# Optimization experiments

Measured on AMD Instinct MI355X. Metric: run time of the kernel, lower is better.

The kernel has to match this reference:

```python
import jax, jax.numpy as jnp
import numpy as np

# ---------- constants ----------
EPS = 1e-5
_rng = np.random.default_rng(0)
_P = _rng.normal(size=(8, 3))
_P /= np.linalg.norm(_P, axis=1, keepdims=True)

def _y2_np(p):
    x, y, z = p[:, 0], p[:, 1], p[:, 2]
    return np.stack([x * y, y * z, 3 * z * z - 1, x * z, x * x - y * y], axis=-1)

_A2 = np.linalg.pinv(_y2_np(_P)).astype(np.float32)  # [5,8]
P_C = jnp.asarray(_P.astype(np.float32))
A2_C = jnp.asarray(_A2)
NORM_CONST = np.float32(1.0 / np.sqrt(20.0))  # avg_num_neighbors ** -0.5
# res update (buffer zeros, not learnable): sigmoid(0)=0.5
_U = 0.5
C_OLD = np.float32(1.0 / np.sqrt(_U * _U + 1.0))
C_NEW = np.float32(_U * C_OLD)


def _y2(p):  # real l=2 monomial basis on unit vectors
    x, y, z = p[..., 0], p[..., 1], p[..., 2]
    return jnp.stack([x * y, y * z, 3.0 * z * z - 1.0, x * z, x * x - y * y], axis=-1)


def _frame(v):  # [E,3] -> R [E,3,3] with R @ v_hat = z
    n = v / jnp.linalg.norm(v, axis=-1, keepdims=True)
    z = jnp.array([0.0, 0.0, 1.0], v.dtype)
    xa = jnp.array([1.0, 0.0, 0.0], v.dtype)
    a = jnp.where(jnp.abs(n[:, 2:3]) < 0.99, z, xa)
    e1 = jnp.cross(a, n)
    e1 = e1 / jnp.linalg.norm(e1, axis=-1, keepdims=True)
    e2 = jnp.cross(n, e1)
    return jnp.stack([e1, e2, n], axis=1)


def _wigner_d2(R):  # [E,3,3] -> D2 [E,5,5] via sample-point fit
    pts = jnp.einsum('pj,eij->epi', P_C, R)  # R @ p_k, [E,8,3]
    M = _y2(pts)  # [E,8,5] = Y_P @ D^T
    Dt = jnp.einsum('ap,epb->eab', A2_C, M)  # [E,5,5]
    return jnp.swapaxes(Dt, 1, 2)


def _sln(x, w0, b0, w1, w2):  # separable equivariant layernorm, 32x0e+16x1e+8x2e
    s = x[:, :32]
    v1 = x[:, 32:80].reshape(-1, 16, 3)
    v2 = x[:, 80:120].reshape(-1, 8, 5)
    mu = jnp.mean(s, axis=-1, keepdims=True)
    var = jnp.mean((s - mu) ** 2, axis=-1, keepdims=True)
    s = (s - mu) * jax.lax.rsqrt(var + EPS) * w0 + b0
    var1 = jnp.mean(v1 ** 2, axis=(1, 2))  # degree-balanced component variance
    var2 = jnp.mean(v2 ** 2, axis=(1, 2))
    inv = jax.lax.rsqrt(0.5 * (var1 + var2) + EPS)[:, None, None]
    v1 = v1 * inv * w1[None, :, None]
    v2 = v2 * inv * w2[None, :, None]
    return jnp.concatenate([s, v1.reshape(-1, 48), v2.reshape(-1, 40)], axis=-1)


def _ir_linear(x, W0, b0, W1, W2):  # irreps-wise linear 32x0e+16x1e+8x2e -> same
    s = x[:, :32] @ (W0 / np.sqrt(32.0)) + b0
    v1 = jnp.einsum('eui,uv->evi', x[:, 32:80].reshape(-1, 16, 3), W1) / np.sqrt(16.0)
    v2 = jnp.einsum('eui,uv->evi', x[:, 80:120].reshape(-1, 8, 5), W2) / np.sqrt(8.0)
    return jnp.concatenate([s, v1.reshape(-1, 48), v2.reshape(-1, 40)], axis=-1)


def _so2(x_cat, R, D2f, D2b, w):  # SO2 linear with per-edge dynamic weights
    E = x_cat.shape[0]
    w0 = w[:, :8960].reshape(E, 112, 80)
    w1r = w[:, 8960:10112].reshape(E, 48, 24)
    w1i = w[:, 10112:11264].reshape(E, 48, 24)
    w2r = w[:, 11264:11392].reshape(E, 16, 8)
    w2i = w[:, 11392:11520].reshape(E, 16, 8)
    # split concatenated [in + hidden] blocks
    s = jnp.concatenate([x_cat[:, :32], x_cat[:, 120:152]], axis=-1)  # [E,64]
    v1 = jnp.concatenate([x_cat[:, 32:80].reshape(E, 16, 3),
                          x_cat[:, 152:200].reshape(E, 16, 3)], axis=1)  # [E,32,3]
    v2 = jnp.concatenate([x_cat[:, 80:120].reshape(E, 8, 5),
                          x_cat[:, 200:240].reshape(E, 16 // 2, 5)], axis=1)  # [E,16,5]
    # rotate into edge-aligned frame
    v1 = jnp.einsum('eij,euj->eui', R, v1)
    v2 = jnp.einsum('eij,euj->eui', D2f, v2)
    in0 = jnp.concatenate([s, v1[:, :, 1], v2[:, :, 2]], axis=-1)   # m=0, [E,112]
    inn1 = jnp.concatenate([v1[:, :, 0], v2[:, :, 1]], axis=-1)     # m=-1, [E,48]
    inp1 = jnp.concatenate([v1[:, :, 2], v2[:, :, 3]], axis=-1)     # m=+1
    inn2 = v2[:, :, 0]  # m=-2
    inp2 = v2[:, :, 4]  # m=+2
    out0 = jnp.einsum('ei,eio->eo', in0, w0) / np.sqrt(112.0)
    op1 = (jnp.einsum('ei,eio->eo', inp1, w1r) - jnp.einsum('ei,eio->eo', inn1, w1i)) / np.sqrt(48.0)
    on1 = (jnp.einsum('ei,eio->eo', inn1, w1r) + jnp.einsum('ei,eio->eo', inp1, w1i)) / np.sqrt(48.0)
    op2 = (jnp.einsum('ei,eio->eo', inp2, w2r) - jnp.einsum('ei,eio->eo', inn2, w2i)) / np.sqrt(16.0)
    on2 = (jnp.einsum('ei,eio->eo', inn2, w2r) + jnp.einsum('ei,eio->eo', inp2, w2i)) / np.sqrt(16.0)
    s_out = out0[:, :56]
    y1 = jnp.stack([on1[:, :16], out0[:, 56:72], op1[:, :16]], axis=-1)  # [E,16,3]
    y2o = jnp.stack([on2, on1[:, 16:24], out0[:, 72:80], op1[:, 16:24], op2], axis=-1)  # [E,8,5]
    # rotate back
    y1 = jnp.einsum('eij,euj->eui', jnp.swapaxes(R, 1, 2), y1)
    y2o = jnp.einsum('eij,euj->eui', D2b, y2o)
    return jnp.concatenate([s_out, y1.reshape(E, 48), y2o.reshape(E, 40)], axis=-1)  # [E,144]


def _gate(m):  # 32x0e scalars | 24x0e gates | 16x1e+8x2e gated
    s = jax.nn.silu(m[:, :32])
    g = jax.nn.sigmoid(m[:, 32:56])
    v1 = m[:, 56:104].reshape(-1, 16, 3) * g[:, :16, None]
    v2 = m[:, 104:144].reshape(-1, 8, 5) * g[:, 16:24, None]
    return jnp.concatenate([s, v1.reshape(-1, 48), v2.reshape(-1, 40)], axis=-1)


def _env(m, we):  # E3ElementLinear: per-mul elementwise weights
    s = m[:, :32] * we[:, :32]
    v1 = m[:, 32:80].reshape(-1, 16, 3) * we[:, 32:48, None]
    v2 = m[:, 80:120].reshape(-1, 8, 5) * we[:, 48:56, None]
    return jnp.concatenate([s, v1.reshape(-1, 48), v2.reshape(-1, 40)], axis=-1)


def setup_inputs() -> dict:
    key = jax.random.key(0)
    ks = jax.random.split(key, 16)
    N, E, L = 512, 10240, 128
    inp = {
        'latents': jax.random.normal(ks[0], (E, L), jnp.float32),
        'node_features': jax.random.normal(ks[1], (N, 120), jnp.float32),
        'hidden_features': jax.random.normal(ks[2], (E, 120), jnp.float32),
        'node_onehot': jnp.ones((N, 16), jnp.float32),
        'edge_vector': jax.random.normal(ks[3], (E, 3), jnp.float32),
        'W_tp': jax.random.normal(ks[4], (L, 11520), jnp.float32),
        'W_env': jax.random.normal(ks[5], (L, 56), jnp.float32),
        'sln_w0': jnp.ones((32,), jnp.float32),
        'sln_b0': jnp.zeros((32,), jnp.float32),
        'sln_w1': jnp.ones((16,), jnp.float32),
        'sln_w2': jnp.ones((8,), jnp.float32),
        'Wp0': jax.random.normal(ks[6], (32, 32), jnp.float32),
        'bp0': jnp.zeros((32,), jnp.float32),
        'Wp1': jax.random.normal(ks[7], (16, 16), jnp.float32),
        'Wp2': jax.random.normal(ks[8], (8, 8), jnp.float32),
        'Wr0': jax.random.normal(ks[9], (32, 32), jnp.float32),
        'br0': jnp.zeros((32,), jnp.float32),
        'Wr1': jax.random.normal(ks[10], (16, 16), jnp.float32),
        'Wr2': jax.random.normal(ks[11], (8, 8), jnp.float32),
        'atom_type': jax.random.randint(ks[12], (N,), 0, 10, jnp.int32),
        'edge_index': jax.random.randint(ks[13], (2, E), 0, N, jnp.int32),
        'active_edges': jnp.arange(E, dtype=jnp.int32),
    }
    return inp


def reference(latents, node_features, hidden_features, node_onehot, edge_vector,
              W_tp, W_env, sln_w0, sln_b0, sln_w1, sln_w2,
              Wp0, bp0, Wp1, Wp2, Wr0, br0, Wr1, Wr2,
              atom_type, edge_index, active_edges):
    n_nodes = node_features.shape[0]
    center = edge_index[0][active_edges]
    nf = _sln(node_features, sln_w0, sln_b0, sln_w1, sln_w2)
    x_cat = jnp.concatenate([nf[center], hidden_features], axis=-1)  # [E,240]
    v = edge_vector[active_edges]
    R = _frame(v)
    D2f = _wigner_d2(R)
    D2b = _wigner_d2(jnp.swapaxes(R, 1, 2))
    wdyn = latents @ (W_tp / np.sqrt(128.0))  # per-edge dynamic SO2 weights
    msg = _so2(x_cat, R, D2f, D2b, wdyn)
    msg = _gate(msg)
    msg = _ir_linear(msg, Wp0, bp0, Wp1, Wp2)
    wenv = latents[active_edges] @ (W_env / np.sqrt(128.0))
    weighted = _env(msg, wenv)
    new_nf = jax.ops.segment_sum(weighted, center, num_segments=n_nodes)
    new_nf = new_nf * NORM_CONST
    res = _ir_linear(node_features, Wr0, br0, Wr1, Wr2)
    return C_NEW * new_nf + C_OLD * res
```

## Files before the change

### kernel.cpp

```cpp
#include <hip/hip_runtime.h>
#include <math.h>

#define E_TOT   10240
#define N_NODES 512
#define NCOL    11520

typedef unsigned short ushort_t;
typedef unsigned int   uint_t;
typedef __bf16 bf16x8 __attribute__((ext_vector_type(8)));
typedef float  f32x4  __attribute__((ext_vector_type(4)));

constexpr float EPSF        = 1e-5f;
constexpr float INV_SQRT128 = 0.08838834764831845f;
constexpr float INV_SQRT112 = 0.09449111825230681f;
constexpr float INV_SQRT48  = 0.14433756729740643f;
constexpr float INV_SQRT32  = 0.17677669529663687f;
constexpr float INV_SQRT16  = 0.25f;
constexpr float INV_SQRT8   = 0.35355339059327373f;
constexpr float SC0 = INV_SQRT128 * INV_SQRT112;
constexpr float SC1 = INV_SQRT128 * INV_SQRT48;
constexpr float SC2 = INV_SQRT128 * INV_SQRT16;
constexpr float C_OLD_ = 0.8944271909999159f;
constexpr float C_NEW_ = 0.4472135954999579f;
constexpr float NORMC  = 0.22360679774997896f;

__device__ __forceinline__ float wsum(float v) {
#pragma unroll
  for (int off = 32; off > 0; off >>= 1) v += __shfl_xor(v, off, 64);
  return v;
}

__device__ __forceinline__ ushort_t f2bf(float x) {
  uint_t u = __float_as_uint(x);
  u = (u + 0x7fffu + ((u >> 16) & 1u)) >> 16;
  return (ushort_t)u;
}

__device__ __forceinline__ void wigner5(const float q[9], float D[25]) {
  const float q0x=q[0],q0y=q[1],q0z=q[2];
  const float q1x=q[3],q1y=q[4],q1z=q[5];
  const float q2x=q[6],q2y=q[7],q2z=q[8];
  D[0]  = q0x*q1y + q1x*q0y;
  D[1]  = q0y*q1z + q1y*q0z;
  D[2]  = 0.5f*(q0z*q1z);
  D[3]  = q0x*q1z + q1x*q0z;
  D[4]  = 0.5f*(q0x*q1x - q0y*q1y);
  D[5]  = q1x*q2y + q2x*q1y;
  D[6]  = q1y*q2z + q2y*q1z;
  D[7]  = 0.5f*(q1z*q2z);
  D[8]  = q1x*q2z + q2x*q1z;
  D[9]  = 0.5f*(q1x*q2x - q1y*q2y);
  D[10] = 6.f*q2x*q2y;
  D[11] = 6.f*q2y*q2z;
  D[12] = 0.5f*(3.f*q2z*q2z - 1.f);
  D[13] = 6.f*q2x*q2z;
  D[14] = 1.5f*(q2x*q2x - q2y*q2y);
  D[15] = q0x*q2y + q2x*q0y;
  D[16] = q0y*q2z + q2y*q0z;
  D[17] = 0.5f*(q0z*q2z);
  D[18] = q0x*q2z + q2x*q0z;
  D[19] = 0.5f*(q0x*q2x - q0y*q2y);
  D[20] = 2.f*(q0x*q0y - q1x*q1y);
  D[21] = 2.f*(q0y*q0z - q1y*q1z);
  D[22] = 0.5f*(q0z*q0z - q1z*q1z);
  D[23] = 2.f*(q0x*q0z - q1x*q1z);
  D[24] = 0.5f*((q0x*q0x - q1x*q1x) - (q0y*q0y - q1y*q1y));
}

__global__ void k0_latpack(const float* __restrict__ lat,
                           ushort_t* __restrict__ lath, ushort_t* __restrict__ latl) {
  int idx = blockIdx.x*256 + threadIdx.x;
  if (idx >= E_TOT*128) return;
  float x = lat[idx];
  ushort_t h = f2bf(x);
  float hf = __uint_as_float(((uint_t)h) << 16);
  lath[idx] = h;
  latl[idx] = f2bf(x - hf);
}

__global__ void k_pack(const float* __restrict__ Wtp, ushort_t* __restrict__ Wp) {
  const int nt = blockIdx.x;
  const int t = threadIdx.x;
  const int kc = t >> 6, lane = t & 63;
  const int m = lane & 15, kg = lane >> 4;
  int col, tt;
  if (nt < 560)      { col = nt/112; tt = nt - col*112; }
  else if (nt < 608) { col = 5;  tt = nt-560; }
  else if (nt < 632) { col = 6;  tt = nt-608; }
  else if (nt < 680) { col = 7;  tt = nt-632; }
  else if (nt < 704) { col = 8;  tt = nt-680; }
  else if (nt < 712) { col = 9;  tt = nt-704; }
  else               { col = 10; tt = nt-712; }
  int c; float sc;
  switch (col) {
    case 5:  c = 8960  + tt*24 + m;                       sc = SC1; break;
    case 6:  c = 8960  + (2*tt + (m>>3))*24 + 16 + (m&7); sc = SC1; break;
    case 7:  c = 10112 + tt*24 + m;                       sc = SC1; break;
    case 8:  c = 10112 + (2*tt + (m>>3))*24 + 16 + (m&7); sc = SC1; break;
    case 9:  c = 11264 + (2*tt + (m>>3))*8 + (m&7);       sc = SC2; break;
    case 10: c = 11392 + (2*tt + (m>>3))*8 + (m&7);       sc = SC2; break;
    default: c = tt*80 + col*16 + m;                      sc = SC0; break;
  }
  ushort_t hi[8], lo[8];
#pragma unroll
  for (int jj = 0; jj < 8; ++jj) {
    int l = kc*32 + kg*8 + jj;
    float w = Wtp[(size_t)l*NCOL + c] * sc;
    ushort_t h = f2bf(w);
    float hf = __uint_as_float(((uint_t)h) << 16);
    hi[jj] = h;
    lo[jj] = f2bf(w - hf);
  }
  size_t base = ((size_t)nt*8 + kc*2)*512 + (size_t)lane*8;
#pragma unroll
  for (int jj = 0; jj < 8; ++jj) {
    Wp[base + jj]       = hi[jj];
    Wp[base + 512 + jj] = lo[jj];
  }
}

__global__ void k1_sln(const float* __restrict__ x_all,
                       const float* __restrict__ w0, const float* __restrict__ b0,
                       const float* __restrict__ w1, const float* __restrict__ w2,
                       float* __restrict__ nf) {
  const int n = blockIdx.x;
  const int t = threadIdx.x;
  const float* x = x_all + n*120;
  float xs = (t < 32) ? x[t] : 0.f;
  float ssum = wsum(xs);
  float ssq  = wsum(xs*xs);
  float mu   = ssum * (1.f/32.f);
  float var  = ssq * (1.f/32.f) - mu*mu;
  float istd = rsqrtf(var + EPSF);
  float q1 = (t < 48) ? x[32+t] : 0.f;
  float v1s = wsum(q1*q1);
  float q2 = (t < 40) ? x[80+t] : 0.f;
  float v2s = wsum(q2*q2);
  float inv = rsqrtf(0.5f*(v1s*(1.f/48.f) + v2s*(1.f/40.f)) + EPSF);
  for (int j = t; j < 120; j += 64) {
    float val = x[j], r;
    if (j < 32)      r = (val - mu)*istd*w0[j] + b0[j];
    else if (j < 80) r = val*inv*w1[(j-32)/3];
    else             r = val*inv*w2[(j-80)/5];
    nf[n*120 + j] = r;
  }
}

__global__ void k2_edge_prep(const float* __restrict__ hid,
                             const float* __restrict__ evec,
                             const int*   __restrict__ eidx,
                             const int*   __restrict__ act,
                             const float* __restrict__ nf,
                             float* __restrict__ invT,
                             float* __restrict__ Rm,
                             float* __restrict__ D2bm) {
  const int e = blockIdx.x*blockDim.x + threadIdx.x;
  if (e >= E_TOT) return;
  const int ae  = act[e];
  const int ctr = eidx[ae];
  float vx = evec[ae*3+0], vy = evec[ae*3+1], vz = evec[ae*3+2];
  float rn = rsqrtf(vx*vx + vy*vy + vz*vz);
  float nx = vx*rn, ny = vy*rn, nz = vz*rn;
  float e1x, e1y, e1z;
  if (fabsf(nz) < 0.99f) { e1x = -ny; e1y = nx;  e1z = 0.f; }
  else                   { e1x = 0.f; e1y = -nz; e1z = ny;  }
  float rl = rsqrtf(e1x*e1x + e1y*e1y + e1z*e1z);
  e1x *= rl; e1y *= rl; e1z *= rl;
  float e2x = ny*e1z - nz*e1y;
  float e2y = nz*e1x - nx*e1z;
  float e2z = nx*e1y - ny*e1x;
  float R[9] = {e1x,e1y,e1z, e2x,e2y,e2z, nx,ny,nz};
#pragma unroll
  for (int j = 0; j < 9; ++j) Rm[e*9 + j] = R[j];
  float Df[25];
  wigner5(R, Df);
  float Rt[9] = {R[0],R[3],R[6], R[1],R[4],R[7], R[2],R[5],R[8]};
  float Db[25];
  wigner5(Rt, Db);
#pragma unroll
  for (int j = 0; j < 25; ++j) D2bm[e*25 + j] = Db[j];
  const float* xa = nf  + (size_t)ctr*120;
  const float* xb = hid + (size_t)e*120;
#define IVST(r_, v_) invT[(size_t)(r_)*E_TOT + e] = (v_)
#pragma unroll
  for (int j = 0; j < 32; ++j) { IVST(j, xa[j]); IVST(32+j, xb[j]); }
#pragma unroll
  for (int u = 0; u < 32; ++u) {
    const float* src = (u < 16) ? (xa + 32 + 3*u) : (xb + 32 + 3*(u-16));
    float px = src[0], py = src[1], pz = src[2];
    float rx = R[0]*px + R[1]*py + R[2]*pz;
    float ry = R[3]*px + R[4]*py + R[5]*pz;
    float rz = R[6]*px + R[7]*py + R[8]*pz;
    IVST(64+u, ry);
    IVST(112+u, rx);
    IVST(160+u, rz);
  }
#pragma unroll
  for (int u = 0; u < 16; ++u) {
    const float* src = (u < 8) ? (xa + 80 + 5*u) : (xb + 80 + 5*(u-8));
    float p0 = src[0], p1 = src[1], p2 = src[2], p3 = src[3], p4 = src[4];
    float d[5];
#pragma unroll
    for (int i = 0; i < 5; ++i)
      d[i] = Df[i*5+0]*p0 + Df[i*5+1]*p1 + Df[i*5+2]*p2 + Df[i*5+3]*p3 + Df[i*5+4]*p4;
    IVST(96+u,  d[2]);
    IVST(144+u, d[1]);
    IVST(192+u, d[3]);
    IVST(208+u, d[0]);
    IVST(224+u, d[4]);
  }
#undef IVST
}

__global__ __launch_bounds__(256)
void k2_wenv(const float* __restrict__ lat, const float* __restrict__ Wenv,
             const int* __restrict__ act, float* __restrict__ wenvo) {
  __shared__ float Wl[128*56];
  __shared__ float latc[256*17];
  __shared__ int   aes[256];
  const int t = threadIdx.x;
  const int e0 = blockIdx.x*256;
  for (int i = t; i < 128*56; i += 256) Wl[i] = Wenv[i];
  aes[t] = act[e0 + t];
  float acc[56];
#pragma unroll
  for (int o = 0; o < 56; ++o) acc[o] = 0.f;
  for (int lc = 0; lc < 8; ++lc) {
    __syncthreads();
    for (int i = t; i < 256*16; i += 256) {
      int el = i >> 4, j = i & 15;
      latc[el*17 + j] = lat[(size_t)aes[el]*128 + lc*16 + j];
    }
    __syncthreads();
#pragma unroll
    for (int j = 0; j < 16; ++j) {
      float lv = latc[t*17 + j];
      const float* wr = &Wl[(lc*16 + j)*56];
#pragma unroll
      for (int o = 0; o < 56; ++o) acc[o] += lv * wr[o];
    }
  }
  float* dst = wenvo + (size_t)(e0 + t)*56;
#pragma unroll
  for (int o = 0; o < 56; ++o) dst[o] = acc[o] * INV_SQRT128;
}

__global__ __launch_bounds__(256, 2)
void k3_gemm(const ushort_t* __restrict__ Wp,
             const ushort_t* __restrict__ lath,
             const ushort_t* __restrict__ latl,
             const float*  __restrict__ invT,
             float* __restrict__ oa_g) {
  __shared__ __align__(16) ushort_t abuf[2][8192];
  const int t = threadIdx.x;
  const int wave = t >> 6, lane = t & 63;
  const int le = lane & 15, g = lane >> 4, gh = g >> 1;
  const int fbase = blockIdx.y * 80;
  const int e0w = blockIdx.x*128 + wave*32;
  bf16x8 Bh[4][2], Bl[4][2];
#pragma unroll
  for (int kc = 0; kc < 4; ++kc)
#pragma unroll
    for (int n = 0; n < 2; ++n) {
      size_t off = (size_t)(e0w + n*16 + le)*128 + kc*32 + g*8;
      Bh[kc][n] = *(const bf16x8*)(lath + off);
      Bl[kc][n] = *(const bf16x8*)(latl + off);
    }
  int col, tt;
  if (fbase < 560)      { col = fbase/112; tt = fbase - col*112; }
  else if (fbase < 608) { col = 5;  tt = fbase-560; }
  else if (fbase < 632) { col = 6;  tt = fbase-608; }
  else if (fbase < 680) { col = 7;  tt = fbase-632; }
  else if (fbase < 704) { col = 8;  tt = fbase-680; }
  else if (fbase < 712) { col = 9;  tt = fbase-704; }
  else                  { col = 10; tt = fbase-712; }
  int mP_, mN_, sP_, sN_, segLen; float sg_; bool PAIR_, TWO_;
  auto setParams = [&](int cf) {
    if (cf < 5)       { segLen=112; mP_=0;   mN_=0;   sP_=cf*16; sN_=0;   sg_=1.f;  PAIR_=false; TWO_=false; }
    else if (cf == 5) { segLen=48;  mP_=160; mN_=112; sP_=80;  sN_=104; sg_=1.f;  PAIR_=false; TWO_=true; }
    else if (cf == 6) { segLen=24;  mP_=160; mN_=112; sP_=96;  sN_=120; sg_=1.f;  PAIR_=true;  TWO_=true; }
    else if (cf == 7) { segLen=48;  mP_=112; mN_=160; sP_=80;  sN_=104; sg_=-1.f; PAIR_=false; TWO_=true; }
    else if (cf == 8) { segLen=24;  mP_=112; mN_=160; sP_=96;  sN_=120; sg_=-1.f; PAIR_=true;  TWO_=true; }
    else if (cf == 9) { segLen=8;   mP_=224; mN_=208; sP_=128; sN_=136; sg_=1.f;  PAIR_=true;  TWO_=true; }
    else              { segLen=8;   mP_=208; mN_=224; sP_=128; sN_=136; sg_=-1.f; PAIR_=true;  TWO_=true; }
  };
  setParams(col);
  f32x4 aP0={0,0,0,0}, aP1={0,0,0,0}, aN0={0,0,0,0}, aN1={0,0,0,0};
  auto flush = [&]() {
#pragma unroll
    for (int r = 0; r < 4; ++r) {
      int mm = g*4 + r;
      int sp = sP_ + (PAIR_ ? (mm & 7) : mm);
      atomicAdd(&oa_g[(size_t)(e0w + le)*144 + sp], sg_*aP0[r]);
      atomicAdd(&oa_g[(size_t)(e0w + 16 + le)*144 + sp], sg_*aP1[r]);
      if (TWO_) {
        int sn = sN_ + (PAIR_ ? (mm & 7) : mm);
        atomicAdd(&oa_g[(size_t)(e0w + le)*144 + sn], aN0[r]);
        atomicAdd(&oa_g[(size_t)(e0w + 16 + le)*144 + sn], aN1[r]);
      }
    }
    aP0 = (f32x4){0,0,0,0}; aP1 = (f32x4){0,0,0,0};
    aN0 = (f32x4){0,0,0,0}; aN1 = (f32x4){0,0,0,0};
  };
#pragma unroll
  for (int qq = 0; qq < 4; ++qq) {
    uint4 v = *(const uint4*)(Wp + ((size_t)fbase*8 + wave*4 + qq)*512 + lane*8);
    *(uint4*)&abuf[0][(wave*4 + qq)*512 + lane*8] = v;
  }
  __syncthreads();
  for (int c = 0; c < 40; ++c) {
    const int cb = c & 1, nb = cb ^ 1;
    uint4 pre[4];
    const bool more = (c + 1) < 40;
    if (more) {
#pragma unroll
      for (int qq = 0; qq < 4; ++qq)
        pre[qq] = *(const uint4*)(Wp + ((size_t)(fbase + 2*(c+1))*8 + wave*4 + qq)*512 + lane*8);
    }
#pragma unroll
    for (int lt = 0; lt < 2; ++lt) {
      int idx = PAIR_ ? (2*tt + gh) : tt;
      int rowP = mP_ + idx;
      float mP0 = invT[(size_t)rowP*E_TOT + e0w + le];
      float mP1 = invT[(size_t)rowP*E_TOT + e0w + 16 + le];
      float mN0 = 0.f, mN1 = 0.f;
      if (TWO_) {
        int rowN = mN_ + idx;
        mN0 = invT[(size_t)rowN*E_TOT + e0w + le];
        mN1 = invT[(size_t)rowN*E_TOT + e0w + 16 + le];
      }
      f32x4 d0 = {0,0,0,0}, d1 = {0,0,0,0};
#pragma unroll
      for (int kc = 0; kc < 4; ++kc) {
        bf16x8 Ah = *(const bf16x8*)&abuf[cb][(lt*8 + kc*2 + 0)*512 + lane*8];
        bf16x8 Al = *(const bf16x8*)&abuf[cb][(lt*8 + kc*2 + 1)*512 + lane*8];
        d0 = __builtin_amdgcn_mfma_f32_16x16x32_bf16(Ah, Bh[kc][0], d0, 0, 0, 0);
        d1 = __builtin_amdgcn_mfma_f32_16x16x32_bf16(Ah, Bh[kc][1], d1, 0, 0, 0);
        d0 = __builtin_amdgcn_mfma_f32_16x16x32_bf16(Ah, Bl[kc][0], d0, 0, 0, 0);
        d1 = __builtin_amdgcn_mfma_f32_16x16x32_bf16(Ah, Bl[kc][1], d1, 0, 0, 0);
        d0 = __builtin_amdgcn_mfma_f32_16x16x32_bf16(Al, Bh[kc][0], d0, 0, 0, 0);
        d1 = __builtin_amdgcn_mfma_f32_16x16x32_bf16(Al, Bh[kc][1], d1, 0, 0, 0);
      }
#pragma unroll
      for (int r = 0; r < 4; ++r) { aP0[r] += mP0*d0[r]; aP1[r] += mP1*d1[r]; }
      if (TWO_) {
#pragma unroll
        for (int r = 0; r < 4; ++r) { aN0[r] += mN0*d0[r]; aN1[r] += mN1*d1[r]; }
      }
      tt++;
      if (tt == segLen) { flush(); col++; tt = 0; setParams(col); }
    }
    if (more) {
#pragma unroll
      for (int qq = 0; qq < 4; ++qq)
        *(uint4*)&abuf[nb][(wave*4 + qq)*512 + lane*8] = pre[qq];
    }
    __syncthreads();
  }
  if (tt > 0) flush();
}

__global__ __launch_bounds__(256)
void k4_epi(const float* __restrict__ oa_g, const float* __restrict__ Rm,
            const float* __restrict__ D2bm, const float* __restrict__ wenvg,
            const int* __restrict__ eidx, const int* __restrict__ act,
            const float* __restrict__ Wp0, const float* __restrict__ bp0,
            const float* __restrict__ Wp1, const float* __restrict__ Wp2,
            float* __restrict__ accg) {
  __shared__ float sc[4][160];
  const int wave = threadIdx.x >> 6, lane = threadIdx.x & 63;
  const int eg = blockIdx.x*4 + wave;
  const float* o_ = oa_g + (size_t)eg*144;
  if (lane < 56) {
    float v = o_[lane];
    sc[wave][lane] = (lane < 32) ? v/(1.f + expf(-v)) : 1.f/(1.f + expf(-v));
  }
  __syncthreads();
  const float* Rr = Rm + (size_t)eg*9;
  const float* Db = D2bm + (size_t)eg*25;
  if (lane < 48) {
    int u = lane/3, cc = lane - u*3;
    float yx = o_[104+u], yy = o_[56+u], yz = o_[80+u];
    float p = Rr[cc]*yx + Rr[3+cc]*yy + Rr[6+cc]*yz;
    sc[wave][56+lane] = p * sc[wave][32+u];
  }
  __syncthreads();
  if (lane < 40) {
    int u = lane/5, ii = lane - u*5;
    float y0 = o_[136+u], y1v = o_[120+u], y2v = o_[72+u], y3 = o_[96+u], y4 = o_[128+u];
    float p = Db[ii*5+0]*y0 + Db[ii*5+1]*y1v + Db[ii*5+2]*y2v + Db[ii*5+3]*y3 + Db[ii*5+4]*y4;
    sc[wave][104+lane] = p * sc[wave][48+u];
  }
  __syncthreads();
  const float* we = wenvg + (size_t)eg*56;
  const int ctr = eidx[act[eg]];
  float* dst = accg + (size_t)ctr*120;
#pragma unroll
  for (int rnd = 0; rnd < 2; ++rnd) {
    int jo = rnd*64 + lane;
    if (jo < 120) {
      float val;
      if (jo < 32) {
        float s = 0.f;
#pragma unroll
        for (int i2 = 0; i2 < 32; ++i2) s += sc[wave][i2]*Wp0[i2*32 + jo];
        val = (s*INV_SQRT32 + bp0[jo]) * we[jo];
      } else if (jo < 80) {
        int jj = jo-32, v = jj/3, cc = jj - v*3;
        float s = 0.f;
#pragma unroll
        for (int u = 0; u < 16; ++u) s += sc[wave][56 + u*3 + cc]*Wp1[u*16 + v];
        val = s*INV_SQRT16*we[32+v];
      } else {
        int jj = jo-80, v = jj/5, ii = jj - v*5;
        float s = 0.f;
#pragma unroll
        for (int u = 0; u < 8; ++u) s += sc[wave][104 + u*5 + ii]*Wp2[u*8 + v];
        val = s*INV_SQRT8*we[48+v];
      }
      atomicAdd(&dst[jo], val);
    }
  }
}

__global__ void k5_final(const float* __restrict__ x_all,
                         const float* __restrict__ Wr0, const float* __restrict__ br0,
                         const float* __restrict__ Wr1, const float* __restrict__ Wr2,
                         const float* __restrict__ accg,
                         float* __restrict__ out) {
  const int n = blockIdx.x;
  const int t = threadIdx.x;
  if (t >= 120) return;
  const float* x = x_all + n*120;
  float r;
  if (t < 32) {
    float s = 0.f;
#pragma unroll
    for (int i = 0; i < 32; ++i) s += x[i]*Wr0[i*32 + t];
    r = s*INV_SQRT32 + br0[t];
  } else if (t < 80) {
    int j = t - 32, v = j/3, cp = j - 3*v;
    float s = 0.f;
#pragma unroll
    for (int u = 0; u < 16; ++u) s += x[32 + u*3 + cp]*Wr1[u*16 + v];
    r = s*INV_SQRT16;
  } else {
    int j = t - 80, v = j/5, cp = j - 5*v;
    float s = 0.f;
#pragma unroll
    for (int u = 0; u < 8; ++u) s += x[80 + u*5 + cp]*Wr2[u*8 + v];
    r = s*INV_SQRT8;
  }
  out[n*120 + t] = C_NEW_*(NORMC*accg[n*120 + t]) + C_OLD_*r;
}

extern "C" void kernel_launch(void* const* d_in, const int* in_sizes, int n_in,
                              void* d_out, int out_size, void* d_ws, size_t ws_size,
                              hipStream_t stream) {
  const float* lat  = (const float*)d_in[0];
  const float* ndf  = (const float*)d_in[1];
  const float* hid  = (const float*)d_in[2];
  const float* evec = (const float*)d_in[4];
  const float* Wtp  = (const float*)d_in[5];
  const float* Wenv = (const float*)d_in[6];
  const float* w0   = (const float*)d_in[7];
  const float* b0   = (const float*)d_in[8];
  const float* w1   = (const float*)d_in[9];
  const float* w2   = (const float*)d_in[10];
  const float* Wp0  = (const float*)d_in[11];
  const float* bp0  = (const float*)d_in[12];
  const float* Wp1  = (const float*)d_in[13];
  const float* Wp2  = (const float*)d_in[14];
  const float* Wr0  = (const float*)d_in[15];
  const float* br0  = (const float*)d_in[16];
  const float* Wr1  = (const float*)d_in[17];
  const float* Wr2  = (const float*)d_in[18];
  const int*   eidx = (const int*)d_in[20];
  const int*   act  = (const int*)d_in[21];
  float* out = (float*)d_out;

  char* p = (char*)d_ws;
  float*    nf    = (float*)(p);
  float*    invT  = (float*)(p + 245760);
  float*    Rm    = (float*)(p + 10076160);
  float*    D2bm  = (float*)(p + 10444800);
  float*    wenv  = (float*)(p + 11468800);
  float*    accg  = (float*)(p + 13762560);
  float*    oa_g  = (float*)(p + 14008320);
  ushort_t* lath  = (ushort_t*)(p + 19906560);
  ushort_t* latl  = (ushort_t*)(p + 22528000);
  ushort_t* Wpack = (ushort_t*)(p + 25149440);

  hipMemsetAsync(accg, 0, 245760, stream);
  hipMemsetAsync(oa_g, 0, 5898240, stream);
  k0_latpack<<<(E_TOT*128 + 255)/256, 256, 0, stream>>>(lat, lath, latl);
  k_pack<<<720, 256, 0, stream>>>(Wtp, Wpack);
  k1_sln<<<N_NODES, 64, 0, stream>>>(ndf, w0, b0, w1, w2, nf);
  k2_edge_prep<<<E_TOT/256, 256, 0, stream>>>(hid, evec, eidx, act, nf, invT, Rm, D2bm);
  k2_wenv<<<E_TOT/256, 256, 0, stream>>>(lat, Wenv, act, wenv);
  k3_gemm<<<dim3(E_TOT/128, 9), 256, 0, stream>>>(Wpack, lath, latl, invT, oa_g);
  k4_epi<<<E_TOT/4, 256, 0, stream>>>(oa_g, Rm, D2bm, wenv, eidx, act, Wp0, bp0, Wp1, Wp2, accg);
  k5_final<<<N_NODES, 128, 0, stream>>>(ndf, Wr0, br0, Wr1, Wr2, accg, out);
}
```

Baseline: 301.3 us.

## Retile SO2 GEMM, stage edge prep via LDS, fuse wenv into epilogue

The SO2 GEMM kernel now gives each wave 64 edges instead of 32 and splits the feature range into 12 chunks of 60 instead of 9 of 80. This reuses each A tile across more MFMAs and issues fewer flush atomics per edge. Edge prep now stages node and hidden features in shared memory and has 8 threads per edge write invT, so stores are coalesced and work is spread across more threads. The separate wenv GEMM kernel is removed and computed per edge inside the epilogue, and the weight-pack stores are vectorised. Trade-offs are higher register pressure in the GEMM and redundant global reads of Wenv in the epilogue.

```diff
diff --git a/kernel.cpp b/kernel.cpp
--- a/kernel.cpp
+++ b/kernel.cpp
@@ -112,11 +112,8 @@
     lo[jj] = f2bf(w - hf);
   }
   size_t base = ((size_t)nt*8 + kc*2)*512 + (size_t)lane*8;
-#pragma unroll
-  for (int jj = 0; jj < 8; ++jj) {
-    Wp[base + jj]       = hi[jj];
-    Wp[base + 512 + jj] = lo[jj];
-  }
+  *(uint4*)&Wp[base]       = *(const uint4*)hi;
+  *(uint4*)&Wp[base + 512] = *(const uint4*)lo;
 }
 
 __global__ void k1_sln(const float* __restrict__ x_all,
@@ -146,103 +143,98 @@
   }
 }
 
-__global__ void k2_edge_prep(const float* __restrict__ hid,
-                             const float* __restrict__ evec,
-                             const int*   __restrict__ eidx,
-                             const int*   __restrict__ act,
-                             const float* __restrict__ nf,
-                             float* __restrict__ invT,
-                             float* __restrict__ Rm,
-                             float* __restrict__ D2bm) {
-  const int e = blockIdx.x*blockDim.x + threadIdx.x;
-  if (e >= E_TOT) return;
-  const int ae  = act[e];
-  const int ctr = eidx[ae];
-  float vx = evec[ae*3+0], vy = evec[ae*3+1], vz = evec[ae*3+2];
-  float rn = rsqrtf(vx*vx + vy*vy + vz*vz);
-  float nx = vx*rn, ny = vy*rn, nz = vz*rn;
-  float e1x, e1y, e1z;
-  if (fabsf(nz) < 0.99f) { e1x = -ny; e1y = nx;  e1z = 0.f; }
-  else                   { e1x = 0.f; e1y = -nz; e1z = ny;  }
-  float rl = rsqrtf(e1x*e1x + e1y*e1y + e1z*e1z);
-  e1x *= rl; e1y *= rl; e1z *= rl;
-  float e2x = ny*e1z - nz*e1y;
-  float e2y = nz*e1x - nx*e1z;
-  float e2z = nx*e1y - ny*e1x;
-  float R[9] = {e1x,e1y,e1z, e2x,e2y,e2z, nx,ny,nz};
-#pragma unroll
-  for (int j = 0; j < 9; ++j) Rm[e*9 + j] = R[j];
-  float Df[25];
-  wigner5(R, Df);
-  float Rt[9] = {R[0],R[3],R[6], R[1],R[4],R[7], R[2],R[5],R[8]};
-  float Db[25];
-  wigner5(Rt, Db);
-#pragma unroll
-  for (int j = 0; j < 25; ++j) D2bm[e*25 + j] = Db[j];
-  const float* xa = nf  + (size_t)ctr*120;
-  const float* xb = hid + (size_t)e*120;
-#define IVST(r_, v_) invT[(size_t)(r_)*E_TOT + e] = (v_)
-#pragma unroll
-  for (int j = 0; j < 32; ++j) { IVST(j, xa[j]); IVST(32+j, xb[j]); }
-#pragma unroll
-  for (int u = 0; u < 32; ++u) {
-    const float* src = (u < 16) ? (xa + 32 + 3*u) : (xb + 32 + 3*(u-16));
-    float px = src[0], py = src[1], pz = src[2];
-    float rx = R[0]*px + R[1]*py + R[2]*pz;
-    float ry = R[3]*px + R[4]*py + R[5]*pz;
-    float rz = R[6]*px + R[7]*py + R[8]*pz;
-    IVST(64+u, ry);
-    IVST(112+u, rx);
-    IVST(160+u, rz);
-  }
-#pragma unroll
-  for (int u = 0; u < 16; ++u) {
-    const float* src = (u < 8) ? (xa + 80 + 5*u) : (xb + 80 + 5*(u-8));
-    float p0 = src[0], p1 = src[1], p2 = src[2], p3 = src[3], p4 = src[4];
-    float d[5];
-#pragma unroll
-    for (int i = 0; i < 5; ++i)
-      d[i] = Df[i*5+0]*p0 + Df[i*5+1]*p1 + Df[i*5+2]*p2 + Df[i*5+3]*p3 + Df[i*5+4]*p4;
-    IVST(96+u,  d[2]);
-    IVST(144+u, d[1]);
-    IVST(192+u, d[3]);
-    IVST(208+u, d[0]);
-    IVST(224+u, d[4]);
-  }
-#undef IVST
-}
-
 __global__ __launch_bounds__(256)
-void k2_wenv(const float* __restrict__ lat, const float* __restrict__ Wenv,
-             const int* __restrict__ act, float* __restrict__ wenvo) {
-  __shared__ float Wl[128*56];
-  __shared__ float latc[256*17];
-  __shared__ int   aes[256];
+void k2_edge_prep(const float* __restrict__ hid,
+                  const float* __restrict__ evec,
+                  const int*   __restrict__ eidx,
+                  const int*   __restrict__ act,
+                  const float* __restrict__ nf,
+                  float* __restrict__ invT,
+                  float* __restrict__ Rm,
+                  float* __restrict__ D2bm) {
+  __shared__ float xs[32][240];
+  __shared__ float Rs[32][9];
+  __shared__ float Dfs[32][25];
+  __shared__ int   ctrs[32];
   const int t = threadIdx.x;
-  const int e0 = blockIdx.x*256;
-  for (int i = t; i < 128*56; i += 256) Wl[i] = Wenv[i];
-  aes[t] = act[e0 + t];
-  float acc[56];
-#pragma unroll
-  for (int o = 0; o < 56; ++o) acc[o] = 0.f;
-  for (int lc = 0; lc < 8; ++lc) {
-    __syncthreads();
-    for (int i = t; i < 256*16; i += 256) {
-      int el = i >> 4, j = i & 15;
-      latc[el*17 + j] = lat[(size_t)aes[el]*128 + lc*16 + j];
-    }
-    __syncthreads();
-#pragma unroll
-    for (int j = 0; j < 16; ++j) {
-      float lv = latc[t*17 + j];
-      const float* wr = &Wl[(lc*16 + j)*56];
-#pragma unroll
-      for (int o = 0; o < 56; ++o) acc[o] += lv * wr[o];
-    }
-  }
-  float* dst = wenvo + (size_t)(e0 + t)*56;
-#pragma unroll
-  for (int o = 0; o < 56; ++o) dst[o] = acc[o] * INV_SQRT128;
+  const int e0 = blockIdx.x*32;
+  if (t < 32) {
+    const int e = e0 + t;
+    const int ae = act[e];
+    ctrs[t] = eidx[ae];
+    float vx = evec[ae*3+0], vy = evec[ae*3+1], vz = evec[ae*3+2];
+    float rn = rsqrtf(vx*vx + vy*vy + vz*vz);
+    float nx = vx*rn, ny = vy*rn, nz = vz*rn;
+    float e1x, e1y, e1z;
+    if (fabsf(nz) < 0.99f) { e1x = -ny; e1y = nx;  e1z = 0.f; }
+    else                   { e1x = 0.f; e1y = -nz; e1z = ny;  }
+    float rl = rsqrtf(e1x*e1x + e1y*e1y + e1z*e1z);
+    e1x *= rl; e1y *= rl; e1z *= rl;
+    float e2x = ny*e1z - nz*e1y;
+    float e2y = nz*e1x - nx*e1z;
+    float e2z = nx*e1y - ny*e1x;
+    float R[9] = {e1x,e1y,e1z, e2x,e2y,e2z, nx,ny,nz};
+#pragma unroll
+    for (int j = 0; j < 9; ++j) { Rs[t][j] = R[j]; Rm[(size_t)e*9 + j] = R[j]; }
+    float Df[25];
+    wigner5(R, Df);
+#pragma unroll
+    for (int j = 0; j < 25; ++j) Dfs[t][j] = Df[j];
+    float Rt[9] = {R[0],R[3],R[6], R[1],R[4],R[7], R[2],R[5],R[8]};
+    float Db[25];
+    wigner5(Rt, Db);
+#pragma unroll
+    for (int j = 0; j < 25; ++j) D2bm[(size_t)e*25 + j] = Db[j];
+  }
+  __syncthreads();
+  for (int i = t; i < 32*120; i += 256) {
+    int s = i/120, j = i - s*120;
+    xs[s][j]     = nf[(size_t)ctrs[s]*120 + j];
+    xs[s][120+j] = hid[(size_t)(e0+s)*120 + j];
+  }
+  __syncthreads();
+  const int e = t & 31, rb = t >> 5;
+  const float* X = xs[e];
+  const float* Rr = Rs[e];
+  const float* Df = Dfs[e];
+#pragma unroll
+  for (int r = rb; r < 240; r += 8) {
+    float val;
+    if (r < 64) {
+      val = (r < 32) ? X[r] : X[120 + r - 32];
+    } else if (r < 96) {
+      int u = r - 64; int b = (u < 16) ? 32 + 3*u : 152 + 3*(u-16);
+      val = Rr[3]*X[b] + Rr[4]*X[b+1] + Rr[5]*X[b+2];
+    } else if (r < 112) {
+      int u = r - 96; int b = (u < 8) ? 80 + 5*u : 200 + 5*(u-8);
+      val = Df[10]*X[b] + Df[11]*X[b+1] + Df[12]*X[b+2] + Df[13]*X[b+3] + Df[14]*X[b+4];
+    } else if (r < 160) {
+      int u = r - 112;
+      if (u < 32) {
+        int b = (u < 16) ? 32 + 3*u : 152 + 3*(u-16);
+        val = Rr[0]*X[b] + Rr[1]*X[b+1] + Rr[2]*X[b+2];
+      } else {
+        int u2 = u - 32; int b = (u2 < 8) ? 80 + 5*u2 : 200 + 5*(u2-8);
+        val = Df[5]*X[b] + Df[6]*X[b+1] + Df[7]*X[b+2] + Df[8]*X[b+3] + Df[9]*X[b+4];
+      }
+    } else if (r < 208) {
+      int u = r - 160;
+      if (u < 32) {
+        int b = (u < 16) ? 32 + 3*u : 152 + 3*(u-16);
+        val = Rr[6]*X[b] + Rr[7]*X[b+1] + Rr[8]*X[b+2];
+      } else {
+        int u2 = u - 32; int b = (u2 < 8) ? 80 + 5*u2 : 200 + 5*(u2-8);
+        val = Df[15]*X[b] + Df[16]*X[b+1] + Df[17]*X[b+2] + Df[18]*X[b+3] + Df[19]*X[b+4];
+      }
+    } else if (r < 224) {
+      int u = r - 208; int b = (u < 8) ? 80 + 5*u : 200 + 5*(u-8);
+      val = Df[0]*X[b] + Df[1]*X[b+1] + Df[2]*X[b+2] + Df[3]*X[b+3] + Df[4]*X[b+4];
+    } else {
+      int u = r - 224; int b = (u < 8) ? 80 + 5*u : 200 + 5*(u-8);
+      val = Df[20]*X[b] + Df[21]*X[b+1] + Df[22]*X[b+2] + Df[23]*X[b+3] + Df[24]*X[b+4];
+    }
+    invT[(size_t)r*E_TOT + e0 + e] = val;
+  }
 }
 
 __global__ __launch_bounds__(256, 2)
@@ -255,13 +247,13 @@
   const int t = threadIdx.x;
   const int wave = t >> 6, lane = t & 63;
   const int le = lane & 15, g = lane >> 4, gh = g >> 1;
-  const int fbase = blockIdx.y * 80;
-  const int e0w = blockIdx.x*128 + wave*32;
-  bf16x8 Bh[4][2], Bl[4][2];
+  const int fbase = blockIdx.y * 60;
+  const int e0w = blockIdx.x*256 + wave*64;
+  bf16x8 Bh[4][4], Bl[4][4];
 #pragma unroll
   for (int kc = 0; kc < 4; ++kc)
 #pragma unroll
-    for (int n = 0; n < 2; ++n) {
+    for (int n = 0; n < 4; ++n) {
       size_t off = (size_t)(e0w + n*16 + le)*128 + kc*32 + g*8;
       Bh[kc][n] = *(const bf16x8*)(lath + off);
       Bl[kc][n] = *(const bf16x8*)(latl + off);
@@ -285,22 +277,24 @@
     else              { segLen=8;   mP_=208; mN_=224; sP_=128; sN_=136; sg_=-1.f; PAIR_=true;  TWO_=true; }
   };
   setParams(col);
-  f32x4 aP0={0,0,0,0}, aP1={0,0,0,0}, aN0={0,0,0,0}, aN1={0,0,0,0};
+  f32x4 aP[4] = {{0,0,0,0},{0,0,0,0},{0,0,0,0},{0,0,0,0}};
+  f32x4 aN[4] = {{0,0,0,0},{0,0,0,0},{0,0,0,0},{0,0,0,0}};
   auto flush = [&]() {
 #pragma unroll
-    for (int r = 0; r < 4; ++r) {
-      int mm = g*4 + r;
-      int sp = sP_ + (PAIR_ ? (mm & 7) : mm);
-      atomicAdd(&oa_g[(size_t)(e0w + le)*144 + sp], sg_*aP0[r]);
-      atomicAdd(&oa_g[(size_t)(e0w + 16 + le)*144 + sp], sg_*aP1[r]);
-      if (TWO_) {
-        int sn = sN_ + (PAIR_ ? (mm & 7) : mm);
-        atomicAdd(&oa_g[(size_t)(e0w + le)*144 + sn], aN0[r]);
-        atomicAdd(&oa_g[(size_t)(e0w + 16 + le)*144 + sn], aN1[r]);
-      }
-    }
-    aP0 = (f32x4){0,0,0,0}; aP1 = (f32x4){0,0,0,0};
-    aN0 = (f32x4){0,0,0,0}; aN1 = (f32x4){0,0,0,0};
+    for (int n = 0; n < 4; ++n) {
+#pragma unroll
+      for (int r = 0; r < 4; ++r) {
+        int mm = g*4 + r;
+        int sp = sP_ + (PAIR_ ? (mm & 7) : mm);
+        atomicAdd(&oa_g[(size_t)(e0w + n*16 + le)*144 + sp], sg_*aP[n][r]);
+        if (TWO_) {
+          int sn = sN_ + (PAIR_ ? (mm & 7) : mm);
+          atomicAdd(&oa_g[(size_t)(e0w + n*16 + le)*144 + sn], aN[n][r]);
+        }
+      }
+      aP[n] = (f32x4){0,0,0,0};
+      aN[n] = (f32x4){0,0,0,0};
+    }
   };
 #pragma unroll
   for (int qq = 0; qq < 4; ++qq) {
@@ -308,10 +302,10 @@
     *(uint4*)&abuf[0][(wave*4 + qq)*512 + lane*8] = v;
   }
   __syncthreads();
-  for (int c = 0; c < 40; ++c) {
+  for (int c = 0; c < 30; ++c) {
     const int cb = c & 1, nb = cb ^ 1;
     uint4 pre[4];
-    const bool more = (c + 1) < 40;
+    const bool more = (c + 1) < 30;
     if (more) {
 #pragma unroll
       for (int qq = 0; qq < 4; ++qq)
@@ -321,31 +315,39 @@
     for (int lt = 0; lt < 2; ++lt) {
       int idx = PAIR_ ? (2*tt + gh) : tt;
       int rowP = mP_ + idx;
-      float mP0 = invT[(size_t)rowP*E_TOT + e0w + le];
-      float mP1 = invT[(size_t)rowP*E_TOT + e0w + 16 + le];
-      float mN0 = 0.f, mN1 = 0.f;
+      float mP[4], mN[4];
+#pragma unroll
+      for (int n = 0; n < 4; ++n)
+        mP[n] = invT[(size_t)rowP*E_TOT + e0w + n*16 + le];
       if (TWO_) {
         int rowN = mN_ + idx;
-        mN0 = invT[(size_t)rowN*E_TOT + e0w + le];
-        mN1 = invT[(size_t)rowN*E_TOT + e0w + 16 + le];
-      }
-      f32x4 d0 = {0,0,0,0}, d1 = {0,0,0,0};
+#pragma unroll
+        for (int n = 0; n < 4; ++n)
+          mN[n] = invT[(size_t)rowN*E_TOT + e0w + n*16 + le];
+      }
+      f32x4 d[4] = {{0,0,0,0},{0,0,0,0},{0,0,0,0},{0,0,0,0}};
 #pragma unroll
       for (int kc = 0; kc < 4; ++kc) {
         bf16x8 Ah = *(const bf16x8*)&abuf[cb][(lt*8 + kc*2 + 0)*512 + lane*8];
         bf16x8 Al = *(const bf16x8*)&abuf[cb][(lt*8 + kc*2 + 1)*512 + lane*8];
-        d0 = __builtin_amdgcn_mfma_f32_16x16x32_bf16(Ah, Bh[kc][0], d0, 0, 0, 0);
-        d1 = __builtin_amdgcn_mfma_f32_16x16x32_bf16(Ah, Bh[kc][1], d1, 0, 0, 0);
-        d0 = __builtin_amdgcn_mfma_f32_16x16x32_bf16(Ah, Bl[kc][0], d0, 0, 0, 0);
-        d1 = __builtin_amdgcn_mfma_f32_16x16x32_bf16(Ah, Bl[kc][1], d1, 0, 0, 0);
-        d0 = __builtin_amdgcn_mfma_f32_16x16x32_bf16(Al, Bh[kc][0], d0, 0, 0, 0);
-        d1 = __builtin_amdgcn_mfma_f32_16x16x32_bf16(Al, Bh[kc][1], d1, 0, 0, 0);
-      }
-#pragma unroll
-      for (int r = 0; r < 4; ++r) { aP0[r] += mP0*d0[r]; aP1[r] += mP1*d1[r]; }
+#pragma unroll
+        for (int n = 0; n < 4; ++n) {
+          d[n] = __builtin_amdgcn_mfma_f32_16x16x32_bf16(Ah, Bh[kc][n], d[n], 0, 0, 0);
+          d[n] = __builtin_amdgcn_mfma_f32_16x16x32_bf16(Ah, Bl[kc][n], d[n], 0, 0, 0);
+          d[n] = __builtin_amdgcn_mfma_f32_16x16x32_bf16(Al, Bh[kc][n], d[n], 0, 0, 0);
+        }
+      }
+#pragma unroll
+      for (int n = 0; n < 4; ++n) {
+#pragma unroll
+        for (int r = 0; r < 4; ++r) aP[n][r] += mP[n]*d[n][r];
+      }
       if (TWO_) {
 #pragma unroll
-        for (int r = 0; r < 4; ++r) { aN0[r] += mN0*d0[r]; aN1[r] += mN1*d1[r]; }
+        for (int n = 0; n < 4; ++n) {
+#pragma unroll
+          for (int r = 0; r < 4; ++r) aN[n][r] += mN[n]*d[n][r];
+        }
       }
       tt++;
       if (tt == segLen) { flush(); col++; tt = 0; setParams(col); }
@@ -362,16 +364,23 @@
 
 __global__ __launch_bounds__(256)
 void k4_epi(const float* __restrict__ oa_g, const float* __restrict__ Rm,
-            const float* __restrict__ D2bm, const float* __restrict__ wenvg,
+            const float* __restrict__ D2bm,
+            const float* __restrict__ lat, const float* __restrict__ Wenv,
             const int* __restrict__ eidx, const int* __restrict__ act,
             const float* __restrict__ Wp0, const float* __restrict__ bp0,
             const float* __restrict__ Wp1, const float* __restrict__ Wp2,
             float* __restrict__ accg) {
-  __shared__ float sc[4][160];
+  __shared__ float sc[4][200];
   const int wave = threadIdx.x >> 6, lane = threadIdx.x & 63;
   const int eg = blockIdx.x*4 + wave;
+  const int ae = act[eg];
   const float* o_ = oa_g + (size_t)eg*144;
   if (lane < 56) {
+    float s = 0.f;
+    const float* lrow = lat + (size_t)ae*128;
+#pragma unroll 4
+    for (int l = 0; l < 128; ++l) s += lrow[l]*Wenv[l*56 + lane];
+    sc[wave][144 + lane] = s * INV_SQRT128;
     float v = o_[lane];
     sc[wave][lane] = (lane < 32) ? v/(1.f + expf(-v)) : 1.f/(1.f + expf(-v));
   }
@@ -392,9 +401,9 @@
     sc[wave][104+lane] = p * sc[wave][48+u];
   }
   __syncthreads();
-  const float* we = wenvg + (size_t)eg*56;
-  const int ctr = eidx[act[eg]];
+  const int ctr = eidx[ae];
   float* dst = accg + (size_t)ctr*120;
+  const float* we = &sc[wave][144];
 #pragma unroll
   for (int rnd = 0; rnd < 2; ++rnd) {
     int jo = rnd*64 + lane;
@@ -484,7 +493,6 @@
   float*    invT  = (float*)(p + 245760);
   float*    Rm    = (float*)(p + 10076160);
   float*    D2bm  = (float*)(p + 10444800);
-  float*    wenv  = (float*)(p + 11468800);
   float*    accg  = (float*)(p + 13762560);
   float*    oa_g  = (float*)(p + 14008320);
   ushort_t* lath  = (ushort_t*)(p + 19906560);
@@ -496,9 +504,9 @@
   k0_latpack<<<(E_TOT*128 + 255)/256, 256, 0, stream>>>(lat, lath, latl);
   k_pack<<<720, 256, 0, stream>>>(Wtp, Wpack);
   k1_sln<<<N_NODES, 64, 0, stream>>>(ndf, w0, b0, w1, w2, nf);
-  k2_edge_prep<<<E_TOT/256, 256, 0, stream>>>(hid, evec, eidx, act, nf, invT, Rm, D2bm);
-  k2_wenv<<<E_TOT/256, 256, 0, stream>>>(lat, Wenv, act, wenv);
-  k3_gemm<<<dim3(E_TOT/128, 9), 256, 0, stream>>>(Wpack, lath, latl, invT, oa_g);
-  k4_epi<<<E_TOT/4, 256, 0, stream>>>(oa_g, Rm, D2bm, wenv, eidx, act, Wp0, bp0, Wp1, Wp2, accg);
+  k2_edge_prep<<<E_TOT/32, 256, 0, stream>>>(hid, evec, eidx, act, nf, invT, Rm, D2bm);
+  k3_gemm<<<dim3(E_TOT/256, 12), 256, 0, stream>>>(Wpack, lath, latl, invT, oa_g);
+  k4_epi<<<E_TOT/4, 256, 0, stream>>>(oa_g, Rm, D2bm, lat, Wenv, eidx, act,
+                                      Wp0, bp0, Wp1, Wp2, accg);
   k5_final<<<N_NODES, 128, 0, stream>>>(ndf, Wr0, br0, Wr1, Wr2, accg, out);
 }
```

Measured after the change: 318.5 us. +5.7%, slower.
